# Optimization experiments

Measured on AMD Instinct MI355X. Metric: run time of the kernel, lower is better.

The kernel has to match this reference:

```python
import jax, jax.numpy as jnp
import numpy as np

B, K, H, W, D = 4, 8, 64, 64, 64
N = H * W


def setup_inputs() -> dict:
    key = jax.random.key(0)
    k1, k2, k3, k4 = jax.random.split(key, 4)
    z = jax.random.uniform(k1, (B, K, H, W), dtype=jnp.float32)  # >0.5 -> bit
    evidence_mask = jax.random.randint(k2, (B, N), 0, 2) > 0
    temperature = jnp.array(1.0, dtype=jnp.float32)
    value_table = jax.random.normal(k3, (2 ** K, D), dtype=jnp.float32)  # nn.Embedding weight
    mask_value = jax.random.normal(k4, (D,), dtype=jnp.float32) * 0.01
    pop_lut = jnp.asarray(np.array([bin(i).count('1') for i in range(256)], dtype=np.float32))
    return {"z": z, "evidence_mask": evidence_mask, "temperature": temperature,
            "value_table": value_table, "mask_value": mask_value, "pop_lut": pop_lut}


def reference(z, evidence_mask, temperature, value_table, mask_value, pop_lut):
    Bz, k, h, w = z.shape
    n = h * w
    # pack k binary planes into byte codes per spatial location
    bits = (z > 0.5).astype(jnp.int32)                          # (B,k,H,W)
    shifts = (2 ** jnp.arange(k, dtype=jnp.int32)).reshape(1, k, 1, 1)
    codes = (bits * shifts).sum(axis=1).reshape(Bz, n)          # (B,N) int in [0,255]
    # Hamming distance via XOR + popcount LUT
    xor = codes[:, :, None] ^ codes[:, None, :]                 # (B,N,N)
    dist = pop_lut[jnp.clip(xor, 0, 255)]                       # (B,N,N) float
    temp = jnp.maximum(temperature, jnp.float32(0.1))
    scores = -dist / temp
    gate = evidence_mask[:, None, :]                            # (B,1,N) -> broadcast over queries
    # masked, NaN-safe softmax (rows with no evidence -> all-zero attn, matching nan fill)
    m = jnp.max(jnp.where(gate, scores, -jnp.inf), axis=-1, keepdims=True)
    m = jnp.where(jnp.isfinite(m), m, jnp.float32(0.0))
    e = jnp.where(gate, jnp.exp(scores - m), jnp.float32(0.0))
    attn = e / jnp.maximum(e.sum(axis=-1, keepdims=True), jnp.float32(1e-20))
    # value gather with mask_value substitution where no evidence
    values = value_table[jnp.clip(codes, 0, 255)]               # (B,N,D)
    values = jnp.where(evidence_mask[:, :, None], values, mask_value)
    out = jnp.einsum('bqk,bkd->bqd', attn, values)              # (B,N,D)
    return out.transpose(0, 2, 1).reshape(Bz, -1, h, w)         # (B,D,H,W)
```

## Files before the change

### kernel.cpp

```cpp
#include <hip/hip_runtime.h>

#define BATCH  4
#define KBITS  8
#define NPOS   4096
#define DDIM   64
#define NCODES 256

__global__ void k_codes_hist(const float* __restrict__ z,
                             const int* __restrict__ evidence_mask,
                             unsigned char* __restrict__ codes,
                             int* __restrict__ hist) {
    const int b  = blockIdx.x >> 4;
    const int n0 = (blockIdx.x & 15) * 256;
    const int tid = threadIdx.x;
    const int n = n0 + tid;

    __shared__ int h[NCODES];
    h[tid] = 0;
    __syncthreads();

    const float* zb = z + (size_t)b * KBITS * NPOS;
    int code = 0;
#pragma unroll
    for (int k = 0; k < KBITS; ++k) {
        code |= (int)(zb[k * NPOS + n] > 0.5f) << k;
    }
    codes[b * NPOS + n] = (unsigned char)code;
    if (evidence_mask[b * NPOS + n] != 0) {
        atomicAdd(&h[code], 1);
    }
    __syncthreads();
    if (h[tid] != 0) atomicAdd(&hist[b * NCODES + tid], h[tid]);
}

__global__ void k_table(const int* __restrict__ hist,
                        const float* __restrict__ value_table,
                        const float* __restrict__ temperature,
                        float* __restrict__ rowg) {
    const int b  = blockIdx.x >> 8;
    const int cq = blockIdx.x & 255;
    const int tid = threadIdx.x;
    const int wv  = tid >> 6;
    const int d   = tid & 63;

    __shared__ float wrow[NCODES];
    __shared__ float accs[4][DDIM];
    __shared__ float dens[4];
    __shared__ int   mns[4];

    const int cnt = hist[b * NCODES + tid];
    const int pop = __popc(cq ^ tid);
    int myMn = (cnt > 0) ? pop : 99;
#pragma unroll
    for (int off = 32; off > 0; off >>= 1) myMn = min(myMn, __shfl_down(myMn, off));
    if (d == 0) mns[wv] = myMn;
    __syncthreads();
    const int mn = min(min(mns[0], mns[1]), min(mns[2], mns[3]));

    const float inv_t = 1.0f / fmaxf(temperature[0], 0.1f);
    wrow[tid] = (mn > KBITS) ? 0.0f
                             : (float)cnt * __expf((float)(mn - pop) * inv_t);
    __syncthreads();

    float acc = 0.0f, den = 0.0f;
#pragma unroll
    for (int i = 0; i < 64; ++i) {
        const int cc = wv * 64 + i;
        const float w = wrow[cc];
        den += w;
        acc = fmaf(w, value_table[cc * DDIM + d], acc);
    }

    accs[wv][d] = acc;
    if (d == 0) dens[wv] = den;
    __syncthreads();
    if (wv == 0) {
        float a  = accs[0][d] + accs[1][d] + accs[2][d] + accs[3][d];
        float dn = dens[0] + dens[1] + dens[2] + dens[3];
        rowg[(((b << 8) + cq) << 6) + d] = a / fmaxf(dn, 1e-20f);
    }
}

__global__ void k_gather(const unsigned char* __restrict__ codes,
                         const float* __restrict__ rowg,
                         float* __restrict__ out) {
    const int gid  = blockIdx.x * 256 + threadIdx.x;
    const int base = gid * 4;
    const int n4   = base & (NPOS - 1);
    const int bd   = base >> 12;
    const int d    = bd & (DDIM - 1);
    const int b    = bd >> 6;

    const uchar4 c4 = *(const uchar4*)(codes + b * NPOS + n4);
    const float* rb = rowg + ((b << 8) << 6) + d;
    float4 o;
    o.x = rb[(int)c4.x << 6];
    o.y = rb[(int)c4.y << 6];
    o.z = rb[(int)c4.z << 6];
    o.w = rb[(int)c4.w << 6];
    *(float4*)(out + base) = o;
}

extern "C" void kernel_launch(void* const* d_in, const int* in_sizes, int n_in,
                              void* d_out, int out_size, void* d_ws, size_t ws_size,
                              hipStream_t stream) {
    const float* z            = (const float*)d_in[0];
    const int*   evidence     = (const int*)d_in[1];
    const float* temperature  = (const float*)d_in[2];
    const float* value_table  = (const float*)d_in[3];

    float* out = (float*)d_out;

    unsigned char* codes = (unsigned char*)d_ws;
    int*           hist  = (int*)((char*)d_ws + 16384);
    float*         rowg  = (float*)((char*)d_ws + 20480);

    hipMemsetAsync(hist, 0, BATCH * NCODES * sizeof(int), stream);
    k_codes_hist<<<BATCH * 16, 256, 0, stream>>>(z, evidence, codes, hist);
    k_table<<<BATCH * NCODES, 256, 0, stream>>>(hist, value_table, temperature, rowg);
    k_gather<<<(BATCH * DDIM * NPOS) / (256 * 4), 256, 0, stream>>>(codes, rowg, out);
}
```

Baseline: 80.92 us.

## Fuse codes, table and gather into one cooperative kernel with grid syncs

Replaces the memset plus three launches with one cooperative kernel of 1024 blocks that runs the code/histogram, per-code row table, and gather phases in order, separated by grid-wide syncs. Per-block histograms are written to a partial buffer and summed in the table phase, which removes the global atomics and the memset. This cuts launch overhead and the gaps between launches. The cost is two grid barriers and a need for all 1024 blocks to be resident at once; if the cooperative launch fails, the old multi-kernel path is used.

```diff
diff --git a/kernel.cpp b/kernel.cpp
--- a/kernel.cpp
+++ b/kernel.cpp
@@ -1,10 +1,116 @@
 #include <hip/hip_runtime.h>
+#include <hip/hip_cooperative_groups.h>
+
+namespace cg = cooperative_groups;
 
 #define BATCH  4
 #define KBITS  8
 #define NPOS   4096
 #define DDIM   64
 #define NCODES 256
+#define NBLK   1024
+
+__global__ __launch_bounds__(256, 4)
+void k_fused(const float* __restrict__ z,
+             const int* __restrict__ evidence_mask,
+             const float* __restrict__ temperature,
+             const float* __restrict__ value_table,
+             unsigned char* __restrict__ codes,
+             int* __restrict__ hist_part,
+             float* __restrict__ rowg,
+             float* __restrict__ out) {
+    const int bi  = blockIdx.x;
+    const int tid = threadIdx.x;
+
+    __shared__ int   h[NCODES];
+    __shared__ float wrow[NCODES];
+    __shared__ float accs[4][DDIM];
+    __shared__ float dens[4];
+    __shared__ int   mns[4];
+
+    cg::grid_group grid = cg::this_grid();
+
+    if (bi < BATCH * 16) {
+        const int b = bi >> 4;
+        const int n = (bi & 15) * 256 + tid;
+        h[tid] = 0;
+        __syncthreads();
+        const float* zb = z + (size_t)b * KBITS * NPOS;
+        int code = 0;
+#pragma unroll
+        for (int k = 0; k < KBITS; ++k)
+            code |= (int)(zb[k * NPOS + n] > 0.5f) << k;
+        codes[b * NPOS + n] = (unsigned char)code;
+        if (evidence_mask[b * NPOS + n] != 0) atomicAdd(&h[code], 1);
+        __syncthreads();
+        hist_part[bi * NCODES + tid] = h[tid];
+    }
+
+    grid.sync();
+
+    {
+        const int b  = bi >> 8;
+        const int cq = bi & 255;
+        const int wv = tid >> 6;
+        const int d  = tid & 63;
+
+        int cnt = 0;
+#pragma unroll
+        for (int j = 0; j < 16; ++j)
+            cnt += hist_part[(b * 16 + j) * NCODES + tid];
+
+        const int pop = __popc(cq ^ tid);
+        int myMn = (cnt > 0) ? pop : 99;
+#pragma unroll
+        for (int off = 32; off > 0; off >>= 1)
+            myMn = min(myMn, __shfl_down(myMn, off));
+        if (d == 0) mns[wv] = myMn;
+        __syncthreads();
+        const int mn = min(min(mns[0], mns[1]), min(mns[2], mns[3]));
+
+        const float inv_t = 1.0f / fmaxf(temperature[0], 0.1f);
+        wrow[tid] = (mn > KBITS) ? 0.0f
+                                 : (float)cnt * __expf((float)(mn - pop) * inv_t);
+        __syncthreads();
+
+        float acc = 0.0f, den = 0.0f;
+#pragma unroll
+        for (int i = 0; i < 64; ++i) {
+            const int cc = wv * 64 + i;
+            const float w = wrow[cc];
+            den += w;
+            acc = fmaf(w, value_table[cc * DDIM + d], acc);
+        }
+        accs[wv][d] = acc;
+        if (d == 0) dens[wv] = den;
+        __syncthreads();
+        if (wv == 0) {
+            float a  = accs[0][d] + accs[1][d] + accs[2][d] + accs[3][d];
+            float dn = dens[0] + dens[1] + dens[2] + dens[3];
+            rowg[(((b << 8) + cq) << 6) + d] = a / fmaxf(dn, 1e-20f);
+        }
+    }
+
+    grid.sync();
+
+    {
+        const int gid  = bi * 256 + tid;
+        const int base = gid * 4;
+        const int n4   = base & (NPOS - 1);
+        const int bd   = base >> 12;
+        const int d    = bd & (DDIM - 1);
+        const int b    = bd >> 6;
+
+        const uchar4 c4 = *(const uchar4*)(codes + b * NPOS + n4);
+        const float* rb = rowg + ((b << 8) << 6) + d;
+        float4 o;
+        o.x = rb[(int)c4.x << 6];
+        o.y = rb[(int)c4.y << 6];
+        o.z = rb[(int)c4.z << 6];
+        o.w = rb[(int)c4.w << 6];
+        *(float4*)(out + base) = o;
+    }
+}
 
 __global__ void k_codes_hist(const float* __restrict__ z,
                              const int* __restrict__ evidence_mask,
@@ -22,13 +128,10 @@
     const float* zb = z + (size_t)b * KBITS * NPOS;
     int code = 0;
 #pragma unroll
-    for (int k = 0; k < KBITS; ++k) {
+    for (int k = 0; k < KBITS; ++k)
         code |= (int)(zb[k * NPOS + n] > 0.5f) << k;
-    }
     codes[b * NPOS + n] = (unsigned char)code;
-    if (evidence_mask[b * NPOS + n] != 0) {
-        atomicAdd(&h[code], 1);
-    }
+    if (evidence_mask[b * NPOS + n] != 0) atomicAdd(&h[code], 1);
     __syncthreads();
     if (h[tid] != 0) atomicAdd(&hist[b * NCODES + tid], h[tid]);
 }
@@ -70,7 +173,6 @@
         den += w;
         acc = fmaf(w, value_table[cc * DDIM + d], acc);
     }
-
     accs[wv][d] = acc;
     if (d == 0) dens[wv] = den;
     __syncthreads();
@@ -104,19 +206,28 @@
 extern "C" void kernel_launch(void* const* d_in, const int* in_sizes, int n_in,
                               void* d_out, int out_size, void* d_ws, size_t ws_size,
                               hipStream_t stream) {
-    const float* z            = (const float*)d_in[0];
-    const int*   evidence     = (const int*)d_in[1];
-    const float* temperature  = (const float*)d_in[2];
-    const float* value_table  = (const float*)d_in[3];
+    const float* z           = (const float*)d_in[0];
+    const int*   evidence    = (const int*)d_in[1];
+    const float* temperature = (const float*)d_in[2];
+    const float* value_table = (const float*)d_in[3];
 
     float* out = (float*)d_out;
 
-    unsigned char* codes = (unsigned char*)d_ws;
-    int*           hist  = (int*)((char*)d_ws + 16384);
-    float*         rowg  = (float*)((char*)d_ws + 20480);
-
-    hipMemsetAsync(hist, 0, BATCH * NCODES * sizeof(int), stream);
-    k_codes_hist<<<BATCH * 16, 256, 0, stream>>>(z, evidence, codes, hist);
-    k_table<<<BATCH * NCODES, 256, 0, stream>>>(hist, value_table, temperature, rowg);
-    k_gather<<<(BATCH * DDIM * NPOS) / (256 * 4), 256, 0, stream>>>(codes, rowg, out);
-}
+    unsigned char* codes     = (unsigned char*)d_ws;
+    int*           hist_part = (int*)((char*)d_ws + 16384);
+    float*         rowg      = (float*)((char*)d_ws + 16384 + 65536);
+
+    void* args[] = {(void*)&z, (void*)&evidence, (void*)&temperature,
+                    (void*)&value_table, (void*)&codes, (void*)&hist_part,
+                    (void*)&rowg, (void*)&out};
+    hipError_t err = hipLaunchCooperativeKernel((const void*)k_fused,
+                                                dim3(NBLK), dim3(256),
+                                                args, 0, stream);
+    if (err != hipSuccess) {
+        int* hist = (int*)((char*)d_ws + 16384);
+        hipMemsetAsync(hist, 0, BATCH * NCODES * sizeof(int), stream);
+        k_codes_hist<<<BATCH * 16, 256, 0, stream>>>(z, evidence, codes, hist);
+        k_table<<<BATCH * NCODES, 256, 0, stream>>>(hist, value_table, temperature, rowg);
+        k_gather<<<(BATCH * DDIM * NPOS) / (256 * 4), 256, 0, stream>>>(codes, rowg, out);
+    }
+}
```

After: 301.5 us. 3.73x slower.

## Fuse code packing, histogram, softmax table and output into one kernel

Applied to the files above, without the earlier changes.

Replaces the memset and three kernels (codes/histogram, per-code softmax table, gather) with one kernel. Each block recomputes the batch's codes and histogram in shared memory with vectorized loads. It then builds softmax weights for 16 query positions, multiplies them against the value table, and writes the output transposed. This removes launch overhead and workspace round-trips, at the cost of every block rereading the whole batch's z and evidence data and doing redundant per-position rather than per-code weighting. The max-subtraction in the softmax is also dropped, which raises some underflow risk at low temperatures.

```diff
diff --git a/kernel.cpp b/kernel.cpp
--- a/kernel.cpp
+++ b/kernel.cpp
@@ -6,117 +6,115 @@
 #define DDIM   64
 #define NCODES 256
 
-__global__ void k_codes_hist(const float* __restrict__ z,
-                             const int* __restrict__ evidence_mask,
-                             unsigned char* __restrict__ codes,
-                             int* __restrict__ hist) {
-    const int b  = blockIdx.x >> 4;
-    const int n0 = (blockIdx.x & 15) * 256;
-    const int tid = threadIdx.x;
-    const int n = n0 + tid;
+__global__ __launch_bounds__(256, 4)
+void k_all(const float* __restrict__ z,
+           const int* __restrict__ evidence_mask,
+           const float* __restrict__ temperature,
+           const float* __restrict__ value_table,
+           float* __restrict__ out) {
+    const int bi    = blockIdx.x;
+    const int b     = bi >> 8;
+    const int chunk = bi & 255;
+    const int tid   = threadIdx.x;
 
-    __shared__ int h[NCODES];
+    __shared__ unsigned int codes_sh[NPOS / 4];
+    __shared__ int   h[NCODES];
+    __shared__ float w_sh[16][NCODES];
+    __shared__ float dens_sh[16];
+    __shared__ float rows_sh[16][DDIM + 1];
+
     h[tid] = 0;
     __syncthreads();
 
-    const float* zb = z + (size_t)b * KBITS * NPOS;
-    int code = 0;
+    const float* zb = z + (size_t)b * (KBITS * NPOS);
+    const int*   eb = evidence_mask + b * NPOS;
 #pragma unroll
-    for (int k = 0; k < KBITS; ++k) {
-        code |= (int)(zb[k * NPOS + n] > 0.5f) << k;
-    }
-    codes[b * NPOS + n] = (unsigned char)code;
-    if (evidence_mask[b * NPOS + n] != 0) {
-        atomicAdd(&h[code], 1);
+    for (int i = 0; i < 4; ++i) {
+        const int p = (i << 10) + (tid << 2);
+        int c0 = 0, c1 = 0, c2 = 0, c3 = 0;
+#pragma unroll
+        for (int k = 0; k < KBITS; ++k) {
+            const float4 v = *(const float4*)(zb + k * NPOS + p);
+            c0 |= (int)(v.x > 0.5f) << k;
+            c1 |= (int)(v.y > 0.5f) << k;
+            c2 |= (int)(v.z > 0.5f) << k;
+            c3 |= (int)(v.w > 0.5f) << k;
+        }
+        codes_sh[(i << 8) + tid] =
+            (unsigned)c0 | ((unsigned)c1 << 8) | ((unsigned)c2 << 16) | ((unsigned)c3 << 24);
+        const int4 e = *(const int4*)(eb + p);
+        if (e.x) atomicAdd(&h[c0], 1);
+        if (e.y) atomicAdd(&h[c1], 1);
+        if (e.z) atomicAdd(&h[c2], 1);
+        if (e.w) atomicAdd(&h[c3], 1);
     }
     __syncthreads();
-    if (h[tid] != 0) atomicAdd(&hist[b * NCODES + tid], h[tid]);
-}
-
-__global__ void k_table(const int* __restrict__ hist,
-                        const float* __restrict__ value_table,
-                        const float* __restrict__ temperature,
-                        float* __restrict__ rowg) {
-    const int b  = blockIdx.x >> 8;
-    const int cq = blockIdx.x & 255;
-    const int tid = threadIdx.x;
-    const int wv  = tid >> 6;
-    const int d   = tid & 63;
-
-    __shared__ float wrow[NCODES];
-    __shared__ float accs[4][DDIM];
-    __shared__ float dens[4];
-    __shared__ int   mns[4];
-
-    const int cnt = hist[b * NCODES + tid];
-    const int pop = __popc(cq ^ tid);
-    int myMn = (cnt > 0) ? pop : 99;
-#pragma unroll
-    for (int off = 32; off > 0; off >>= 1) myMn = min(myMn, __shfl_down(myMn, off));
-    if (d == 0) mns[wv] = myMn;
-    __syncthreads();
-    const int mn = min(min(mns[0], mns[1]), min(mns[2], mns[3]));
 
     const float inv_t = 1.0f / fmaxf(temperature[0], 0.1f);
-    wrow[tid] = (mn > KBITS) ? 0.0f
-                             : (float)cnt * __expf((float)(mn - pop) * inv_t);
+    const float cntf  = (float)h[tid];
+#pragma unroll
+    for (int j = 0; j < 16; ++j) {
+        const int cq = (codes_sh[(chunk << 2) + (j >> 2)] >> ((j & 3) << 3)) & 255;
+        w_sh[j][tid] = cntf * __expf((float)__popc(cq ^ tid) * -inv_t);
+    }
     __syncthreads();
 
-    float acc = 0.0f, den = 0.0f;
+    {
+        const int j  = tid >> 4;
+        const int c0 = tid & 15;
+        float s = 0.0f;
 #pragma unroll
-    for (int i = 0; i < 64; ++i) {
-        const int cc = wv * 64 + i;
-        const float w = wrow[cc];
-        den += w;
-        acc = fmaf(w, value_table[cc * DDIM + d], acc);
+        for (int i = 0; i < 16; ++i) s += w_sh[j][c0 + (i << 4)];
+#pragma unroll
+        for (int m = 1; m < 16; m <<= 1) s += __shfl_xor(s, m, 16);
+        if (c0 == 0) dens_sh[j] = fmaxf(s, 1e-20f);
     }
+    __syncthreads();
 
-    accs[wv][d] = acc;
-    if (d == 0) dens[wv] = den;
+    const int wv = tid >> 6;
+    const int d  = tid & 63;
+    float acc0 = 0.0f, acc1 = 0.0f, acc2 = 0.0f, acc3 = 0.0f;
+    const float* vt = value_table + d;
+    for (int c = 0; c < NCODES; c += 4) {
+        const float v0 = vt[(c + 0) << 6];
+        const float v1 = vt[(c + 1) << 6];
+        const float v2 = vt[(c + 2) << 6];
+        const float v3 = vt[(c + 3) << 6];
+        const float4 wa = *(const float4*)&w_sh[wv     ][c];
+        const float4 wb = *(const float4*)&w_sh[wv + 4 ][c];
+        const float4 wc = *(const float4*)&w_sh[wv + 8 ][c];
+        const float4 wd = *(const float4*)&w_sh[wv + 12][c];
+        acc0 = fmaf(wa.x, v0, fmaf(wa.y, v1, fmaf(wa.z, v2, fmaf(wa.w, v3, acc0))));
+        acc1 = fmaf(wb.x, v0, fmaf(wb.y, v1, fmaf(wb.z, v2, fmaf(wb.w, v3, acc1))));
+        acc2 = fmaf(wc.x, v0, fmaf(wc.y, v1, fmaf(wc.z, v2, fmaf(wc.w, v3, acc2))));
+        acc3 = fmaf(wd.x, v0, fmaf(wd.y, v1, fmaf(wd.z, v2, fmaf(wd.w, v3, acc3))));
+    }
+    rows_sh[wv     ][d] = acc0 / dens_sh[wv     ];
+    rows_sh[wv + 4 ][d] = acc1 / dens_sh[wv + 4 ];
+    rows_sh[wv + 8 ][d] = acc2 / dens_sh[wv + 8 ];
+    rows_sh[wv + 12][d] = acc3 / dens_sh[wv + 12];
     __syncthreads();
-    if (wv == 0) {
-        float a  = accs[0][d] + accs[1][d] + accs[2][d] + accs[3][d];
-        float dn = dens[0] + dens[1] + dens[2] + dens[3];
-        rowg[(((b << 8) + cq) << 6) + d] = a / fmaxf(dn, 1e-20f);
+
+    float* ob = out + (size_t)b * DDIM * NPOS + (chunk << 4);
+#pragma unroll
+    for (int it = 0; it < 4; ++it) {
+        const int idx = (it << 8) + tid;
+        const int j   = idx & 15;
+        const int dd  = idx >> 4;
+        ob[(size_t)dd * NPOS + j] = rows_sh[j][dd];
     }
-}
-
-__global__ void k_gather(const unsigned char* __restrict__ codes,
-                         const float* __restrict__ rowg,
-                         float* __restrict__ out) {
-    const int gid  = blockIdx.x * 256 + threadIdx.x;
-    const int base = gid * 4;
-    const int n4   = base & (NPOS - 1);
-    const int bd   = base >> 12;
-    const int d    = bd & (DDIM - 1);
-    const int b    = bd >> 6;
-
-    const uchar4 c4 = *(const uchar4*)(codes + b * NPOS + n4);
-    const float* rb = rowg + ((b << 8) << 6) + d;
-    float4 o;
-    o.x = rb[(int)c4.x << 6];
-    o.y = rb[(int)c4.y << 6];
-    o.z = rb[(int)c4.z << 6];
-    o.w = rb[(int)c4.w << 6];
-    *(float4*)(out + base) = o;
 }
 
 extern "C" void kernel_launch(void* const* d_in, const int* in_sizes, int n_in,
                               void* d_out, int out_size, void* d_ws, size_t ws_size,
                               hipStream_t stream) {
-    const float* z            = (const float*)d_in[0];
-    const int*   evidence     = (const int*)d_in[1];
-    const float* temperature  = (const float*)d_in[2];
-    const float* value_table  = (const float*)d_in[3];
+    const float* z           = (const float*)d_in[0];
+    const int*   evidence    = (const int*)d_in[1];
+    const float* temperature = (const float*)d_in[2];
+    const float* value_table = (const float*)d_in[3];
 
     float* out = (float*)d_out;
 
-    unsigned char* codes = (unsigned char*)d_ws;
-    int*           hist  = (int*)((char*)d_ws + 16384);
-    float*         rowg  = (float*)((char*)d_ws + 20480);
-
-    hipMemsetAsync(hist, 0, BATCH * NCODES * sizeof(int), stream);
-    k_codes_hist<<<BATCH * 16, 256, 0, stream>>>(z, evidence, codes, hist);
-    k_table<<<BATCH * NCODES, 256, 0, stream>>>(hist, value_table, temperature, rowg);
-    k_gather<<<(BATCH * DDIM * NPOS) / (256 * 4), 256, 0, stream>>>(codes, rowg, out);
+    k_all<<<BATCH * 256, 256, 0, stream>>>(z, evidence, temperature,
+                                           value_table, out);
 }
```

New measurement: 83.52 us. 1.03x slower.

## Replace per-row softmax table with Hamming-kernel butterfly transform over codes

Applied to the files above, without the earlier changes.

Because exp(-popcount(a^b)/T) factorizes into a product of per-bit factors r = exp(-1/T), the weighted sum over all 256 codes for every query code becomes an 8-stage butterfly. Four stages run within each thread's registers and four through wavefront shuffles. This replaces the 256x256x64 dense table build with one 1024-thread block per batch. It also swaps the global atomic histogram and its memset for per-block partial histograms that are summed in the new kernel. The max-subtraction stabilisation is dropped and relies on the normaliser cancelling the scale. Only 4 blocks run for the table stage, so that stage uses very few CUs.

```diff
diff --git a/kernel.cpp b/kernel.cpp
--- a/kernel.cpp
+++ b/kernel.cpp
@@ -9,11 +9,10 @@
 __global__ void k_codes_hist(const float* __restrict__ z,
                              const int* __restrict__ evidence_mask,
                              unsigned char* __restrict__ codes,
-                             int* __restrict__ hist) {
+                             int* __restrict__ hist_part) {
     const int b  = blockIdx.x >> 4;
-    const int n0 = (blockIdx.x & 15) * 256;
+    const int n  = (blockIdx.x & 15) * 256 + threadIdx.x;
     const int tid = threadIdx.x;
-    const int n = n0 + tid;
 
     __shared__ int h[NCODES];
     h[tid] = 0;
@@ -22,62 +21,78 @@
     const float* zb = z + (size_t)b * KBITS * NPOS;
     int code = 0;
 #pragma unroll
-    for (int k = 0; k < KBITS; ++k) {
+    for (int k = 0; k < KBITS; ++k)
         code |= (int)(zb[k * NPOS + n] > 0.5f) << k;
-    }
     codes[b * NPOS + n] = (unsigned char)code;
-    if (evidence_mask[b * NPOS + n] != 0) {
-        atomicAdd(&h[code], 1);
+    if (evidence_mask[b * NPOS + n] != 0) atomicAdd(&h[code], 1);
+    __syncthreads();
+    hist_part[blockIdx.x * NCODES + tid] = h[tid];
+}
+
+__global__ __launch_bounds__(1024)
+void k_butterfly(const int* __restrict__ hist_part,
+                 const float* __restrict__ value_table,
+                 const float* __restrict__ temperature,
+                 float* __restrict__ rowg) {
+    const int b   = blockIdx.x;
+    const int tid = threadIdx.x;
+
+    __shared__ float cnt_sh[NCODES];
+    if (tid < NCODES) {
+        int s = 0;
+#pragma unroll
+        for (int j = 0; j < 16; ++j)
+            s += hist_part[(b * 16 + j) * NCODES + tid];
+        cnt_sh[tid] = (float)s;
     }
     __syncthreads();
-    if (h[tid] != 0) atomicAdd(&hist[b * NCODES + tid], h[tid]);
-}
 
-__global__ void k_table(const int* __restrict__ hist,
-                        const float* __restrict__ value_table,
-                        const float* __restrict__ temperature,
-                        float* __restrict__ rowg) {
-    const int b  = blockIdx.x >> 8;
-    const int cq = blockIdx.x & 255;
-    const int tid = threadIdx.x;
-    const int wv  = tid >> 6;
-    const int d   = tid & 63;
+    const int l   = tid & 63;
+    const int w   = tid >> 6;
+    const int d   = (w << 2) | (l >> 4);
+    const int clo = l & 15;
+    const float r = __expf(-1.0f / fmaxf(temperature[0], 0.1f));
 
-    __shared__ float wrow[NCODES];
-    __shared__ float accs[4][DDIM];
-    __shared__ float dens[4];
-    __shared__ int   mns[4];
-
-    const int cnt = hist[b * NCODES + tid];
-    const int pop = __popc(cq ^ tid);
-    int myMn = (cnt > 0) ? pop : 99;
+    float g[16], nn[16];
 #pragma unroll
-    for (int off = 32; off > 0; off >>= 1) myMn = min(myMn, __shfl_down(myMn, off));
-    if (d == 0) mns[wv] = myMn;
-    __syncthreads();
-    const int mn = min(min(mns[0], mns[1]), min(mns[2], mns[3]));
-
-    const float inv_t = 1.0f / fmaxf(temperature[0], 0.1f);
-    wrow[tid] = (mn > KBITS) ? 0.0f
-                             : (float)cnt * __expf((float)(mn - pop) * inv_t);
-    __syncthreads();
-
-    float acc = 0.0f, den = 0.0f;
-#pragma unroll
-    for (int i = 0; i < 64; ++i) {
-        const int cc = wv * 64 + i;
-        const float w = wrow[cc];
-        den += w;
-        acc = fmaf(w, value_table[cc * DDIM + d], acc);
+    for (int i = 0; i < 16; ++i) {
+        const int c  = clo | (i << 4);
+        const float cf = cnt_sh[c];
+        nn[i] = cf;
+        g[i]  = cf * value_table[(c << 6) | d];
     }
 
-    accs[wv][d] = acc;
-    if (d == 0) dens[wv] = den;
-    __syncthreads();
-    if (wv == 0) {
-        float a  = accs[0][d] + accs[1][d] + accs[2][d] + accs[3][d];
-        float dn = dens[0] + dens[1] + dens[2] + dens[3];
-        rowg[(((b << 8) + cq) << 6) + d] = a / fmaxf(dn, 1e-20f);
+#pragma unroll
+    for (int k = 0; k < 4; ++k) {
+        const int m = 1 << k;
+#pragma unroll
+        for (int i = 0; i < 16; ++i) {
+            if ((i & m) == 0) {
+                const int j = i | m;
+                const float a = g[i],  bb = g[j];
+                g[i]  = fmaf(r, bb, a);  g[j]  = fmaf(r, a, bb);
+                const float na = nn[i], nb = nn[j];
+                nn[i] = fmaf(r, nb, na); nn[j] = fmaf(r, na, nb);
+            }
+        }
+    }
+#pragma unroll
+    for (int k = 0; k < 4; ++k) {
+        const int m = 1 << k;
+#pragma unroll
+        for (int i = 0; i < 16; ++i) {
+            const float o  = __shfl_xor(g[i],  m);
+            g[i]  = fmaf(r, o, g[i]);
+            const float on = __shfl_xor(nn[i], m);
+            nn[i] = fmaf(r, on, nn[i]);
+        }
+    }
+
+    float* rb = rowg + ((size_t)b << 14);
+#pragma unroll
+    for (int i = 0; i < 16; ++i) {
+        const int c = clo | (i << 4);
+        rb[(c << 6) | d] = g[i] / fmaxf(nn[i], 1e-20f);
     }
 }
 
@@ -92,7 +107,7 @@
     const int b    = bd >> 6;
 
     const uchar4 c4 = *(const uchar4*)(codes + b * NPOS + n4);
-    const float* rb = rowg + ((b << 8) << 6) + d;
+    const float* rb = rowg + ((size_t)b << 14) + d;
     float4 o;
     o.x = rb[(int)c4.x << 6];
     o.y = rb[(int)c4.y << 6];
@@ -104,19 +119,18 @@
 extern "C" void kernel_launch(void* const* d_in, const int* in_sizes, int n_in,
                               void* d_out, int out_size, void* d_ws, size_t ws_size,
                               hipStream_t stream) {
-    const float* z            = (const float*)d_in[0];
-    const int*   evidence     = (const int*)d_in[1];
-    const float* temperature  = (const float*)d_in[2];
-    const float* value_table  = (const float*)d_in[3];
+    const float* z           = (const float*)d_in[0];
+    const int*   evidence    = (const int*)d_in[1];
+    const float* temperature = (const float*)d_in[2];
+    const float* value_table = (const float*)d_in[3];
 
     float* out = (float*)d_out;
 
-    unsigned char* codes = (unsigned char*)d_ws;
-    int*           hist  = (int*)((char*)d_ws + 16384);
-    float*         rowg  = (float*)((char*)d_ws + 20480);
+    unsigned char* codes     = (unsigned char*)d_ws;
+    int*           hist_part = (int*)((char*)d_ws + 16384);
+    float*         rowg      = (float*)((char*)d_ws + 16384 + 65536);
 
-    hipMemsetAsync(hist, 0, BATCH * NCODES * sizeof(int), stream);
-    k_codes_hist<<<BATCH * 16, 256, 0, stream>>>(z, evidence, codes, hist);
-    k_table<<<BATCH * NCODES, 256, 0, stream>>>(hist, value_table, temperature, rowg);
+    k_codes_hist<<<BATCH * 16, 256, 0, stream>>>(z, evidence, codes, hist_part);
+    k_butterfly<<<BATCH, 1024, 0, stream>>>(hist_part, value_table, temperature, rowg);
     k_gather<<<(BATCH * DDIM * NPOS) / (256 * 4), 256, 0, stream>>>(codes, rowg, out);
 }
```

Result: slower. 83.96 us (+3.8%).
